# Performance work log

Measured on AMD Instinct MI355X. Metric: run time of the kernel, lower is better.

## Reference

```python
import jax, jax.numpy as jnp
import numpy as np

B, N, E, H = 16, 1024, 1024, 16  # batch must equal num_heads due to the 'hbkd' einsum in the original
D = E // H


def setup_inputs() -> dict:
    key = jax.random.key(0)
    ks = jax.random.split(key, 9)
    s = 0.02
    return {
        "x": jax.random.normal(ks[0], (B, N, E), dtype=jnp.float32),
        "Wq": jax.random.normal(ks[1], (E, E), dtype=jnp.float32) * s,
        "bq": jax.random.normal(ks[2], (E,), dtype=jnp.float32) * s,
        "Wk": jax.random.normal(ks[3], (E, E), dtype=jnp.float32) * s,
        "bk": jax.random.normal(ks[4], (E,), dtype=jnp.float32) * s,
        "Wv": jax.random.normal(ks[5], (E, E), dtype=jnp.float32) * s,
        "bv": jax.random.normal(ks[6], (E,), dtype=jnp.float32) * s,
        "Wp": jax.random.normal(ks[7], (E, E), dtype=jnp.float32) * s,
        "bp": jax.random.normal(ks[8], (E,), dtype=jnp.float32) * s,
    }


def _split_heads(t):  # [b, n, (h d)] -> [b, h, n, d]
    b, n, e = t.shape
    return t.reshape(b, n, H, D).transpose(0, 2, 1, 3)


def reference(x, Wq, bq, Wk, bk, Wv, bv, Wp, bp):
    q = _split_heads(x @ Wq.T + bq)  # [b, h, n, d]
    k = _split_heads(x @ Wk.T + bk)
    v = _split_heads(x @ Wv.T + bv)
    # Faithful to original: K is contracted with its batch/head axes SWAPPED ('hbkd').
    energy = jnp.einsum('bhqd,hbkd->bhqk', q, k)  # [b, h, n, n]
    # Faithful: softmax over the HEAD axis (dim=1), scale applied AFTER softmax.
    scale = E ** 0.5
    att = jax.nn.softmax(energy, axis=1) / scale
    # dropout rate is 0.0 -> identity
    o = jnp.einsum('bhal,bhlv->bhav', att, v)  # [b, h, n, d]
    o = o.transpose(0, 2, 1, 3).reshape(B, N, E)  # [b, n, (h d)]
    return o @ Wp.T + bp
```

## Files before the change

### kernel.cpp

```cpp
#include <hip/hip_runtime.h>
#include <hip/hip_bf16.h>

#define DEVI __device__ __forceinline__

typedef float f32x4 __attribute__((ext_vector_type(4)));
typedef short bf16x8 __attribute__((ext_vector_type(8)));
typedef unsigned short u16x4 __attribute__((ext_vector_type(4)));


DEVI unsigned short f2bf(float f) {
  union { float f; unsigned u; } v; v.f = f;
  unsigned r = v.u + 0x7fffu + ((v.u >> 16) & 1u);
  return (unsigned short)(r >> 16);
}

DEVI float fexp2(float x) {
#if __has_builtin(__builtin_amdgcn_exp2f)
  return __builtin_amdgcn_exp2f(x);
#else
  return exp2f(x);
#endif
}

DEVI float frcp(float x) {
#if __has_builtin(__builtin_amdgcn_rcpf)
  return __builtin_amdgcn_rcpf(x);
#else
  return 1.0f / x;
#endif
}

DEVI unsigned cvtpk(float a, float b) {
  unsigned r;
  asm("v_cvt_pk_bf16_f32 %0, %1, %2" : "=v"(r) : "v"(a), "v"(b));
  return r;
}

DEVI void gload_lds16(const unsigned short* g, unsigned short* l) {
  __builtin_amdgcn_global_load_lds(
      (const __attribute__((address_space(1))) void*)g,
      (__attribute__((address_space(3))) void*)l, 16, 0, 0);
}

DEVI void wg_barrier() {
  asm volatile("s_waitcnt lgkmcnt(0)" ::: "memory");
  __builtin_amdgcn_s_barrier();
  __builtin_amdgcn_sched_barrier(0);
}

__global__ void cvt_kernel(const float* __restrict__ s, unsigned short* __restrict__ d, int n4) {
  int i = blockIdx.x * blockDim.x + threadIdx.x;
  const int st = gridDim.x * blockDim.x;
  for (; i < n4; i += st) {
    const float4 v = reinterpret_cast<const float4*>(s)[i];
    u16x4 o;
    o[0] = f2bf(v.x); o[1] = f2bf(v.y); o[2] = f2bf(v.z); o[3] = f2bf(v.w);
    reinterpret_cast<u16x4*>(d)[i] = o;
  }
}

DEVI void gemm_tile(const unsigned short* __restrict__ A,
                    const unsigned short* __restrict__ Bw,
                    int m0, int n0,
                    unsigned short* lsA, unsigned short* lsB,
                    f32x4 acc[4][4]) {
  const int tid = threadIdx.x;
  const int w = tid >> 6, l = tid & 63, lg = l >> 4, lr = l & 15;
  const int wr = w >> 1, wc = w & 1;
  for (int kt = 0; kt < 1024; kt += 64) {
#pragma unroll
    for (int i = 0; i < 4; i++) {
      const int c = i * 256 + tid;
      const int row = c >> 3, col = (c & 7) * 8;
      gload_lds16(&A[(m0 + row) * 1024 + kt + col], &lsA[(i * 256 + w * 64) * 8]);
      gload_lds16(&Bw[(n0 + row) * 1024 + kt + col], &lsB[(i * 256 + w * 64) * 8]);
    }
    __syncthreads();
#pragma unroll
    for (int ks = 0; ks < 2; ks++) {
      bf16x8 af[4], bf_[4];
#pragma unroll
      for (int fi = 0; fi < 4; fi++) af[fi] = *(const bf16x8*)&lsA[(wr * 64 + fi * 16 + lr) * 64 + ks * 32 + lg * 8];
#pragma unroll
      for (int fj = 0; fj < 4; fj++) bf_[fj] = *(const bf16x8*)&lsB[(wc * 64 + fj * 16 + lr) * 64 + ks * 32 + lg * 8];
#pragma unroll
      for (int fi = 0; fi < 4; fi++)
#pragma unroll
        for (int fj = 0; fj < 4; fj++)
          acc[fi][fj] = __builtin_amdgcn_mfma_f32_16x16x32_bf16(af[fi], bf_[fj], acc[fi][fj], 0, 0, 0);
    }
    __syncthreads();
  }
}

__global__ __launch_bounds__(256, 2) void proj_qkv(
    const unsigned short* __restrict__ X, const unsigned short* __restrict__ W3,
    const float* __restrict__ bq, const float* __restrict__ bk, const float* __restrict__ bv,
    unsigned short* __restrict__ outq, unsigned short* __restrict__ outk, unsigned short* __restrict__ outv) {
  __shared__ unsigned short lsA[128 * 64];
  __shared__ unsigned short lsB[128 * 64];
  const int z = blockIdx.z;
  const int m0 = blockIdx.x * 128, n0 = blockIdx.y * 128;
  const unsigned short* Bw = W3 + z * 1048576;
  f32x4 acc[4][4];
  const f32x4 z4 = {0.f, 0.f, 0.f, 0.f};
#pragma unroll
  for (int i = 0; i < 4; i++)
#pragma unroll
    for (int j = 0; j < 4; j++) acc[i][j] = z4;
  gemm_tile(X, Bw, m0, n0, lsA, lsB, acc);

  const int tid = threadIdx.x;
  const int w = tid >> 6, l = tid & 63, lg = l >> 4, lr = l & 15, wr = w >> 1, wc = w & 1;
  const float* bias = (z == 0) ? bq : ((z == 1) ? bk : bv);
  const float SC = 1.4426950408889634f;
#pragma unroll
  for (int fi = 0; fi < 4; fi++) {
    const int mb = m0 + wr * 64 + fi * 16 + lg * 4;
#pragma unroll
    for (int fj = 0; fj < 4; fj++) {
      const int ncol = n0 + wc * 64 + fj * 16 + lr;
      const float bsv = bias[ncol];
      const int h = ncol >> 6, d = ncol & 63;
      if (z == 0) {
        const int ks = d >> 5, lgq = (d >> 3) & 3, eq = d & 7;
#pragma unroll
        for (int r = 0; r < 4; r++) {
          const int m = mb + r;
          const int bb = m >> 10, nr = m & 1023;
          const int nt = nr >> 4, lrq = nr & 15;
          const int idx = (((bb * 64 + nt) * 32 + h * 2 + ks) * 64 + lgq * 16 + lrq) * 8 + eq;
          outq[idx] = f2bf((acc[fi][fj][r] + bsv) * SC);
        }
      } else if (z == 1) {
        const int ks = d >> 5, lhi = ((d >> 3) & 3) * 16, eq = d & 7;
#pragma unroll
        for (int r = 0; r < 4; r++) {
          const int m = mb + r;
          const int n = m & 1023, bx = m >> 10;
          const int lane = lhi + (n & 15);
          const int idx = ((((h * 64 + (n >> 4)) * 16 + bx) * 2 + ks) * 64 + lane) * 8 + eq;
          outk[idx] = f2bf(acc[fi][fj][r] + bsv);
        }
      } else {
        const int dt = d >> 4, lrv = d & 15;
        const int bb = mb >> 10, n = mb & 1023;
        const int kc = n >> 5, lgv = (n >> 3) & 3, ev = n & 7;
        u16x4 pk;
#pragma unroll
        for (int r = 0; r < 4; r++) pk[r] = f2bf(acc[fi][fj][r] + bsv);
        const int idx0 = ((((bb * 16 + h) * 32 + kc) * 4 + dt) * 64 + lgv * 16 + lrv) * 8 + ev;
        *(u16x4*)&outv[idx0] = pk;
      }
    }
  }
}

__global__ __launch_bounds__(256, 2) void proj_out(
    const unsigned short* __restrict__ A, const unsigned short* __restrict__ Wp,
    const float* __restrict__ bias, float* __restrict__ out) {
  __shared__ unsigned short lsA[128 * 64];
  __shared__ unsigned short lsB[128 * 64];
  const int m0 = blockIdx.x * 128, n0 = blockIdx.y * 128;
  f32x4 acc[4][4];
  const f32x4 z4 = {0.f, 0.f, 0.f, 0.f};
#pragma unroll
  for (int i = 0; i < 4; i++)
#pragma unroll
    for (int j = 0; j < 4; j++) acc[i][j] = z4;
  gemm_tile(A, Wp, m0, n0, lsA, lsB, acc);
  const int tid = threadIdx.x;
  const int w = tid >> 6, l = tid & 63, lg = l >> 4, lr = l & 15, wr = w >> 1, wc = w & 1;
#pragma unroll
  for (int fi = 0; fi < 4; fi++) {
    const int mb = m0 + wr * 64 + fi * 16 + lg * 4;
#pragma unroll
    for (int fj = 0; fj < 4; fj++) {
      const int ncol = n0 + wc * 64 + fj * 16 + lr;
      const float bsv = bias[ncol];
#pragma unroll
      for (int r = 0; r < 4; r++) out[(mb + r) * 1024 + ncol] = acc[fi][fj][r] + bsv;
    }
  }
}

#define ATTN_BODY(IT, KC, KN)                                                  \
  {                                                                            \
    int qo = 0;                                                                \
    asm volatile("" : "+v"(qo));                                               \
    f32x4 e[4][2];                                                             \
    _Pragma("unroll") for (int hl = 0; hl < 4; hl++) {                         \
      const int h = hq * 4 + hl;                                               \
      _Pragma("unroll") for (int qh = 0; qh < 2; qh++) {                       \
        bf16x8 q0 = *(const bf16x8*)((const char*)qlds + qo + (qh * 32 + h * 2 + 0) * 1024 + l * 16); \
        bf16x8 q1 = *(const bf16x8*)((const char*)qlds + qo + (qh * 32 + h * 2 + 1) * 1024 + l * 16); \
        f32x4 t = __builtin_amdgcn_mfma_f32_16x16x32_bf16(KC[hl * 2 + 0], q0, z4, 0, 0, 0); \
        t = __builtin_amdgcn_mfma_f32_16x16x32_bf16(KC[hl * 2 + 1], q1, t, 0, 0, 0); \
        t[0] = fexp2(t[0]); t[1] = fexp2(t[1]); t[2] = fexp2(t[2]); t[3] = fexp2(t[3]); \
        e[hl][qh] = t;                                                         \
      }                                                                        \
    }                                                                          \
    {                                                                          \
      const unsigned short* knp = kroot + (size_t)((((IT) + 1) & 15) * 4) * 16384; \
      _Pragma("unroll") for (int i = 0; i < 8; i++) KN[i] = *(const bf16x8*)(knp + i * 512); \
    }                                                                          \
    f32x4 s0 = (e[0][0] + e[1][0]) + (e[2][0] + e[3][0]);                      \
    f32x4 s1 = (e[0][1] + e[1][1]) + (e[2][1] + e[3][1]);                      \
    *(f32x4*)&sumbuf[((ksub * 4 + hq) * 2 + 0) * 256 + l * 4] = s0;            \
    *(f32x4*)&sumbuf[((ksub * 4 + hq) * 2 + 1) * 256 + l * 4] = s1;            \
    wg_barrier();                                                              \
    _Pragma("unroll") for (int p = 1; p < 4; p++) {                            \
      const int hqp = hq ^ p;                                                  \
      s0 += *(const f32x4*)&sumbuf[((ksub * 4 + hqp) * 2 + 0) * 256 + l * 4];  \
      s1 += *(const f32x4*)&sumbuf[((ksub * 4 + hqp) * 2 + 1) * 256 + l * 4];  \
    }                                                                          \
    f32x4 inv0, inv1;                                                          \
    inv0[0] = frcp(s0[0]) * 0.03125f; inv0[1] = frcp(s0[1]) * 0.03125f;        \
    inv0[2] = frcp(s0[2]) * 0.03125f; inv0[3] = frcp(s0[3]) * 0.03125f;        \
    inv1[0] = frcp(s1[0]) * 0.03125f; inv1[1] = frcp(s1[1]) * 0.03125f;        \
    inv1[2] = frcp(s1[2]) * 0.03125f; inv1[3] = frcp(s1[3]) * 0.03125f;        \
    _Pragma("unroll") for (int hl = 0; hl < 4; hl++) {                         \
      const int h = hq * 4 + hl;                                               \
      _Pragma("unroll") for (int qh = 0; qh < 2; qh++) {                       \
        f32x4 vv = e[hl][qh] * (qh ? inv1 : inv0);                             \
        uint2 pk;                                                              \
        pk.x = cvtpk(vv[0], vv[1]);                                            \
        pk.y = cvtpk(vv[2], vv[3]);                                            \
        *(uint2*)((char*)abuf + h * 4096 + (qh * 16 + lr) * 128 + ((kpart ^ wswz) << 1)) = pk; \
      }                                                                        \
    }                                                                          \
    {                                                                          \
      const unsigned short* vbp = vroot + (size_t)((IT) * 2) * 2048;           \
      _Pragma("unroll") for (int kst = 0; kst < 2; kst++)                      \
        _Pragma("unroll") for (int dt = 0; dt < 4; dt++)                       \
          vr[kst * 4 + dt] = *(const bf16x8*)(vbp + kst * 2048 + dt * 512);    \
    }                                                                          \
    wg_barrier();                                                              \
    bf16x8 pa[2][2];                                                           \
    _Pragma("unroll") for (int qt = 0; qt < 2; qt++)                           \
      _Pragma("unroll") for (int kst = 0; kst < 2; kst++)                      \
        pa[qt][kst] = *(const bf16x8*)((const char*)abuf + w * 4096 + qt * 2048 + lr * 128 + (((kst * 4 + lg) ^ (lr & 7)) << 4)); \
    _Pragma("unroll") for (int qt = 0; qt < 2; qt++)                           \
      _Pragma("unroll") for (int kst = 0; kst < 2; kst++)                      \
        _Pragma("unroll") for (int dt = 0; dt < 4; dt++)                       \
          oacc[qt][dt] = __builtin_amdgcn_mfma_f32_16x16x32_bf16(pa[qt][kst], vr[kst * 4 + dt], oacc[qt][dt], 0, 0, 0); \
  }

__global__ __launch_bounds__(1024, 4) void attn5(
    const unsigned short* __restrict__ Q2,
    const unsigned short* __restrict__ K2,
    const unsigned short* __restrict__ V2,
    unsigned short* __restrict__ O) {
  __shared__ unsigned short qlds[32768];
  __shared__ unsigned short abuf[32768];
  __shared__ float sumbuf[8192];

  const int tid = threadIdx.x;
  const int w = tid >> 6, l = tid & 63;
  const int lr = l & 15, lg = l >> 4;
  const int bid = blockIdx.x;
  const int swz = (bid & 7) * 64 + (bid >> 3);
  const int b = swz >> 5, qt32 = swz & 31;
  const int ksub = w & 3, hq = w >> 2;

  {
    const unsigned short* qsrc = Q2 + (size_t)(b * 64 + qt32 * 2) * 16384 + tid * 8;
    unsigned short* qdst = qlds + tid * 8;
#pragma unroll
    for (int r = 0; r < 4; r++) gload_lds16(qsrc + r * 8192, qdst + r * 8192);
  }

  const int kpart = ksub * 16 + lg * 4;
  const int wswz = (lr & 7) << 3;

  const f32x4 z4 = {0.f, 0.f, 0.f, 0.f};
  f32x4 oacc[2][4];
#pragma unroll
  for (int qt = 0; qt < 2; qt++)
#pragma unroll
    for (int dt = 0; dt < 4; dt++) oacc[qt][dt] = z4;

  const unsigned short* kroot = K2 + (size_t)(b * 64 + ksub) * 16384 + hq * 4096 + l * 8;
  const unsigned short* vroot = V2 + (size_t)((b * 16 + w) * 32) * 2048 + l * 8;

  bf16x8 kA[8], kB[8], vr[8];
#pragma unroll
  for (int i = 0; i < 8; i++) kA[i] = *(const bf16x8*)(kroot + i * 512);

  asm volatile("s_waitcnt vmcnt(0) lgkmcnt(0)" ::: "memory");
  __builtin_amdgcn_s_barrier();
  __builtin_amdgcn_sched_barrier(0);

#pragma unroll 1
  for (int it2 = 0; it2 < 8; it2++) {
    ATTN_BODY(it2 * 2, kA, kB)
    ATTN_BODY(it2 * 2 + 1, kB, kA)
  }

#pragma unroll
  for (int qt = 0; qt < 2; qt++)
#pragma unroll
    for (int dt = 0; dt < 4; dt++)
#pragma unroll
      for (int r = 0; r < 4; r++) {
        const int n = qt32 * 32 + qt * 16 + lg * 4 + r;
        O[(size_t)(b * 1024 + n) * 1024 + w * 64 + dt * 16 + lr] = f2bf(oacc[qt][dt][r]);
      }
}

extern "C" void kernel_launch(void* const* d_in, const int* in_sizes, int n_in,
                              void* d_out, int out_size, void* d_ws, size_t ws_size,
                              hipStream_t stream) {
  const float* x  = (const float*)d_in[0];
  const float* Wq = (const float*)d_in[1];
  const float* bq = (const float*)d_in[2];
  const float* Wk = (const float*)d_in[3];
  const float* bk = (const float*)d_in[4];
  const float* Wv = (const float*)d_in[5];
  const float* bv = (const float*)d_in[6];
  const float* Wp = (const float*)d_in[7];
  const float* bp = (const float*)d_in[8];

  char* ws = (char*)d_ws;
  unsigned short* xbf  = (unsigned short*)(ws);
  unsigned short* qbf  = (unsigned short*)(ws + 33554432);
  unsigned short* kbf  = (unsigned short*)(ws + 67108864);
  unsigned short* vtbf = (unsigned short*)(ws + 100663296);
  unsigned short* wbf  = (unsigned short*)(ws + 134217728);

  cvt_kernel<<<2048, 256, 0, stream>>>(x, xbf, 4194304);
  cvt_kernel<<<512, 256, 0, stream>>>(Wq, wbf, 262144);
  cvt_kernel<<<512, 256, 0, stream>>>(Wk, wbf + 1048576, 262144);
  cvt_kernel<<<512, 256, 0, stream>>>(Wv, wbf + 2097152, 262144);
  cvt_kernel<<<512, 256, 0, stream>>>(Wp, wbf + 3145728, 262144);

  proj_qkv<<<dim3(128, 8, 3), 256, 0, stream>>>(xbf, wbf, bq, bk, bv, qbf, kbf, vtbf);
  attn5<<<512, 1024, 0, stream>>>(qbf, kbf, vtbf, xbf);
  proj_out<<<dim3(128, 8, 1), 256, 0, stream>>>(xbf, wbf + 3145728, bp, (float*)d_out);
}
```

Measured before the change: 350.3 us.

## Software-pipeline attention loop: overlap PV MFMA of previous tile with next energy phase

Restructures the attention kernel loop so the P·V matrix multiply for iteration it-1 is issued alongside the QK energy/exp phase of iteration it, with a prologue and epilogue. K fragments are now loaded just-in-time inside the energy phase instead of double-buffered in registers, and V is loaded at the start of each iteration. PV MFMAs get raised wave priority via s_setprio. This aims to hide barrier and latency stalls between the softmax reduction and PV, but direct K loads may expose global-memory latency that the old register double-buffering hid.

```diff
diff --git a/kernel.cpp b/kernel.cpp
--- a/kernel.cpp
+++ b/kernel.cpp
@@ -184,31 +184,32 @@
   }
 }
 
-#define ATTN_BODY(IT, KC, KN)                                                  \
+#define E_PHASE(IT)                                                            \
   {                                                                            \
     int qo = 0;                                                                \
     asm volatile("" : "+v"(qo));                                               \
-    f32x4 e[4][2];                                                             \
+    const unsigned short* kp = kroot + (size_t)(IT) * 65536;                   \
     _Pragma("unroll") for (int hl = 0; hl < 4; hl++) {                         \
       const int h = hq * 4 + hl;                                               \
+      bf16x8 k0 = *(const bf16x8*)(kp + (hl * 2 + 0) * 512);                   \
+      bf16x8 k1 = *(const bf16x8*)(kp + (hl * 2 + 1) * 512);                   \
       _Pragma("unroll") for (int qh = 0; qh < 2; qh++) {                       \
         bf16x8 q0 = *(const bf16x8*)((const char*)qlds + qo + (qh * 32 + h * 2 + 0) * 1024 + l * 16); \
         bf16x8 q1 = *(const bf16x8*)((const char*)qlds + qo + (qh * 32 + h * 2 + 1) * 1024 + l * 16); \
-        f32x4 t = __builtin_amdgcn_mfma_f32_16x16x32_bf16(KC[hl * 2 + 0], q0, z4, 0, 0, 0); \
-        t = __builtin_amdgcn_mfma_f32_16x16x32_bf16(KC[hl * 2 + 1], q1, t, 0, 0, 0); \
+        f32x4 t = __builtin_amdgcn_mfma_f32_16x16x32_bf16(k0, q0, z4, 0, 0, 0); \
+        t = __builtin_amdgcn_mfma_f32_16x16x32_bf16(k1, q1, t, 0, 0, 0);       \
         t[0] = fexp2(t[0]); t[1] = fexp2(t[1]); t[2] = fexp2(t[2]); t[3] = fexp2(t[3]); \
         e[hl][qh] = t;                                                         \
       }                                                                        \
     }                                                                          \
-    {                                                                          \
-      const unsigned short* knp = kroot + (size_t)((((IT) + 1) & 15) * 4) * 16384; \
-      _Pragma("unroll") for (int i = 0; i < 8; i++) KN[i] = *(const bf16x8*)(knp + i * 512); \
-    }                                                                          \
-    f32x4 s0 = (e[0][0] + e[1][0]) + (e[2][0] + e[3][0]);                      \
-    f32x4 s1 = (e[0][1] + e[1][1]) + (e[2][1] + e[3][1]);                      \
+    s0 = (e[0][0] + e[1][0]) + (e[2][0] + e[3][0]);                            \
+    s1 = (e[0][1] + e[1][1]) + (e[2][1] + e[3][1]);                            \
     *(f32x4*)&sumbuf[((ksub * 4 + hq) * 2 + 0) * 256 + l * 4] = s0;            \
     *(f32x4*)&sumbuf[((ksub * 4 + hq) * 2 + 1) * 256 + l * 4] = s1;            \
-    wg_barrier();                                                              \
+  }
+
+#define FINISH_PHASE()                                                         \
+  {                                                                            \
     _Pragma("unroll") for (int p = 1; p < 4; p++) {                            \
       const int hqp = hq ^ p;                                                  \
       s0 += *(const f32x4*)&sumbuf[((ksub * 4 + hqp) * 2 + 0) * 256 + l * 4];  \
@@ -229,24 +230,33 @@
         *(uint2*)((char*)abuf + h * 4096 + (qh * 16 + lr) * 128 + ((kpart ^ wswz) << 1)) = pk; \
       }                                                                        \
     }                                                                          \
-    {                                                                          \
-      const unsigned short* vbp = vroot + (size_t)((IT) * 2) * 2048;           \
-      _Pragma("unroll") for (int kst = 0; kst < 2; kst++)                      \
-        _Pragma("unroll") for (int dt = 0; dt < 4; dt++)                       \
-          vr[kst * 4 + dt] = *(const bf16x8*)(vbp + kst * 2048 + dt * 512);    \
-    }                                                                          \
-    wg_barrier();                                                              \
-    bf16x8 pa[2][2];                                                           \
+  }
+
+#define V_LOAD(IT)                                                             \
+  {                                                                            \
+    const unsigned short* vbp = vroot + (size_t)(IT) * 4096;                   \
+    _Pragma("unroll") for (int f = 0; f < 8; f++)                              \
+      vr[f] = *(const bf16x8*)(vbp + f * 512);                                 \
+  }
+
+#define PA_LOAD()                                                              \
+  {                                                                            \
     _Pragma("unroll") for (int qt = 0; qt < 2; qt++)                           \
       _Pragma("unroll") for (int kst = 0; kst < 2; kst++)                      \
-        pa[qt][kst] = *(const bf16x8*)((const char*)abuf + w * 4096 + qt * 2048 + lr * 128 + (((kst * 4 + lg) ^ (lr & 7)) << 4)); \
+        pa[qt * 2 + kst] = *(const bf16x8*)((const char*)abuf + w * 4096 + qt * 2048 + lr * 128 + (((kst * 4 + lg) ^ (lr & 7)) << 4)); \
+  }
+
+#define PV_PHASE()                                                             \
+  {                                                                            \
+    __builtin_amdgcn_s_setprio(1);                                             \
     _Pragma("unroll") for (int qt = 0; qt < 2; qt++)                           \
       _Pragma("unroll") for (int kst = 0; kst < 2; kst++)                      \
         _Pragma("unroll") for (int dt = 0; dt < 4; dt++)                       \
-          oacc[qt][dt] = __builtin_amdgcn_mfma_f32_16x16x32_bf16(pa[qt][kst], vr[kst * 4 + dt], oacc[qt][dt], 0, 0, 0); \
-  }
-
-__global__ __launch_bounds__(1024, 4) void attn5(
+          oacc[qt][dt] = __builtin_amdgcn_mfma_f32_16x16x32_bf16(pa[qt * 2 + kst], vr[kst * 4 + dt], oacc[qt][dt], 0, 0, 0); \
+    __builtin_amdgcn_s_setprio(0);                                             \
+  }
+
+__global__ __launch_bounds__(1024, 4) void attn6(
     const unsigned short* __restrict__ Q2,
     const unsigned short* __restrict__ K2,
     const unsigned short* __restrict__ V2,
@@ -283,19 +293,33 @@
   const unsigned short* kroot = K2 + (size_t)(b * 64 + ksub) * 16384 + hq * 4096 + l * 8;
   const unsigned short* vroot = V2 + (size_t)((b * 16 + w) * 32) * 2048 + l * 8;
 
-  bf16x8 kA[8], kB[8], vr[8];
-#pragma unroll
-  for (int i = 0; i < 8; i++) kA[i] = *(const bf16x8*)(kroot + i * 512);
+  f32x4 e[4][2];
+  f32x4 s0, s1;
+  bf16x8 vr[8], pa[4];
 
   asm volatile("s_waitcnt vmcnt(0) lgkmcnt(0)" ::: "memory");
   __builtin_amdgcn_s_barrier();
   __builtin_amdgcn_sched_barrier(0);
 
+  E_PHASE(0)
+  wg_barrier();
+  FINISH_PHASE()
+  wg_barrier();
+  PA_LOAD()
+
 #pragma unroll 1
-  for (int it2 = 0; it2 < 8; it2++) {
-    ATTN_BODY(it2 * 2, kA, kB)
-    ATTN_BODY(it2 * 2 + 1, kB, kA)
-  }
+  for (int it = 1; it < 16; it++) {
+    V_LOAD(it - 1)
+    E_PHASE(it)
+    PV_PHASE()
+    wg_barrier();
+    FINISH_PHASE()
+    wg_barrier();
+    PA_LOAD()
+  }
+
+  V_LOAD(15)
+  PV_PHASE()
 
 #pragma unroll
   for (int qt = 0; qt < 2; qt++)
@@ -335,6 +359,6 @@
   cvt_kernel<<<512, 256, 0, stream>>>(Wp, wbf + 3145728, 262144);
 
   proj_qkv<<<dim3(128, 8, 3), 256, 0, stream>>>(xbf, wbf, bq, bk, bv, qbf, kbf, vtbf);
-  attn5<<<512, 1024, 0, stream>>>(qbf, kbf, vtbf, xbf);
+  attn6<<<512, 1024, 0, stream>>>(qbf, kbf, vtbf, xbf);
   proj_out<<<dim3(128, 8, 1), 256, 0, stream>>>(xbf, wbf + 3145728, bp, (float*)d_out);
 }
```

Result: slower. 391.0 us (+11.6%).

## Rewrite projection GEMMs as 256x256 double-buffered, swizzled, pipelined tiles

Applied to the files above, without the earlier changes.

Replaces the 128x128 single-buffered GEMM tile used by the QKV and output projections with a 256x256 tile computed by 512 threads. Global-to-LDS loads for the next K-step are interleaved with MFMA phases across two LDS buffers, gated by vmcnt waits and s_setprio. An XOR swizzle on LDS columns is meant to avoid bank conflicts. The goal is to hide memory latency and raise arithmetic intensity, at the cost of 128 KB of LDS per block, higher register pressure and fewer blocks in the grid.

```diff
diff --git a/kernel.cpp b/kernel.cpp
--- a/kernel.cpp
+++ b/kernel.cpp
@@ -59,67 +59,111 @@
   }
 }
 
-DEVI void gemm_tile(const unsigned short* __restrict__ A,
-                    const unsigned short* __restrict__ Bw,
-                    int m0, int n0,
-                    unsigned short* lsA, unsigned short* lsB,
-                    f32x4 acc[4][4]) {
+
+#define STA(BUF, C, K0) gload_lds16(&A[(size_t)(m0 + (C)*64 + srow) * 1024 + (K0) + scol], &lsA[BUF][(C)*4096 + tid*8])
+#define STB(BUF, C, K0) gload_lds16(&Bw[(size_t)(n0 + (C)*64 + srow) * 1024 + (K0) + scol], &lsB[BUF][(C)*4096 + tid*8])
+
+#define DSREAD_A(BUF, MF, KS) (*(const bf16x8*)&lsA[BUF][arow + (MF)*1024 + ((KS) ? sx1 : sx0)])
+#define DSREAD_B(BUF, NF, KS) (*(const bf16x8*)&lsB[BUF][brow + (NF)*1024 + ((KS) ? sx1 : sx0)])
+
+#define MFMA16(P, AF)                                                          \
+    __builtin_amdgcn_s_setprio(1);                                             \
+    _Pragma("unroll") for (int mfi = 0; mfi < 2; mfi++)                        \
+      _Pragma("unroll") for (int nf = 0; nf < 4; nf++)                         \
+        _Pragma("unroll") for (int ks = 0; ks < 2; ks++)                       \
+          acc[2*(P)+mfi][nf] = __builtin_amdgcn_mfma_f32_16x16x32_bf16(        \
+              AF[mfi][ks], bfr[nf][ks], acc[2*(P)+mfi][nf], 0, 0, 0);          \
+    __builtin_amdgcn_s_setprio(0);
+
+#define PHASE(BUF, P, LB, STG)                                                 \
+  { __builtin_amdgcn_s_barrier();                                              \
+    bf16x8 af[2][2];                                                           \
+    _Pragma("unroll") for (int i = 0; i < 2; i++)                              \
+      _Pragma("unroll") for (int k2 = 0; k2 < 2; k2++)                         \
+        af[i][k2] = DSREAD_A(BUF, 2*(P)+i, k2);                                \
+    if (LB) {                                                                  \
+      _Pragma("unroll") for (int n2 = 0; n2 < 4; n2++)                         \
+        _Pragma("unroll") for (int k2 = 0; k2 < 2; k2++)                       \
+          bfr[n2][k2] = DSREAD_B(BUF, n2, k2);                                 \
+    }                                                                          \
+    STG;                                                                       \
+    MFMA16(P, af) }
+
+#define GSTEP(CB, NB, K1)                                                      \
+    asm volatile("s_waitcnt vmcnt(2)" ::: "memory");                           \
+    PHASE(CB, 0, 1, { STB(NB,0,K1); STB(NB,1,K1); })                           \
+    PHASE(CB, 1, 0, { STB(NB,2,K1); STB(NB,3,K1); })                           \
+    asm volatile("s_waitcnt vmcnt(4)" ::: "memory");                           \
+    PHASE(CB, 2, 0, { STA(NB,0,K1); STA(NB,2,K1); })                           \
+    PHASE(CB, 3, 0, { STA(NB,1,K1); STA(NB,3,K1); })
+
+DEVI void gemm256_main(const unsigned short* __restrict__ A,
+                       const unsigned short* __restrict__ Bw,
+                       int m0, int n0,
+                       unsigned short (&lsA)[2][16384],
+                       unsigned short (&lsB)[2][16384],
+                       f32x4 (&acc)[8][4]) {
   const int tid = threadIdx.x;
-  const int w = tid >> 6, l = tid & 63, lg = l >> 4, lr = l & 15;
-  const int wr = w >> 1, wc = w & 1;
-  for (int kt = 0; kt < 1024; kt += 64) {
-#pragma unroll
-    for (int i = 0; i < 4; i++) {
-      const int c = i * 256 + tid;
-      const int row = c >> 3, col = (c & 7) * 8;
-      gload_lds16(&A[(m0 + row) * 1024 + kt + col], &lsA[(i * 256 + w * 64) * 8]);
-      gload_lds16(&Bw[(n0 + row) * 1024 + kt + col], &lsB[(i * 256 + w * 64) * 8]);
-    }
-    __syncthreads();
-#pragma unroll
-    for (int ks = 0; ks < 2; ks++) {
-      bf16x8 af[4], bf_[4];
-#pragma unroll
-      for (int fi = 0; fi < 4; fi++) af[fi] = *(const bf16x8*)&lsA[(wr * 64 + fi * 16 + lr) * 64 + ks * 32 + lg * 8];
-#pragma unroll
-      for (int fj = 0; fj < 4; fj++) bf_[fj] = *(const bf16x8*)&lsB[(wc * 64 + fj * 16 + lr) * 64 + ks * 32 + lg * 8];
-#pragma unroll
-      for (int fi = 0; fi < 4; fi++)
-#pragma unroll
-        for (int fj = 0; fj < 4; fj++)
-          acc[fi][fj] = __builtin_amdgcn_mfma_f32_16x16x32_bf16(af[fi], bf_[fj], acc[fi][fj], 0, 0, 0);
-    }
-    __syncthreads();
-  }
-}
-
-__global__ __launch_bounds__(256, 2) void proj_qkv(
-    const unsigned short* __restrict__ X, const unsigned short* __restrict__ W3,
+  const int l = tid & 63, lr = l & 15, lg = l >> 4;
+  const int w = tid >> 6, wm = w >> 2, wn = w & 3;
+  const int srow = tid >> 3;
+  const int scol = (((tid & 7) ^ (srow & 7)) * 8);
+  const int sx0 = (lg * 8) ^ ((lr & 7) << 3);
+  const int sx1 = (32 + lg * 8) ^ ((lr & 7) << 3);
+  const int arow = (wm * 128 + lr) * 64;
+  const int brow = (wn * 64 + lr) * 64;
+
+  STB(0,0,0); STB(0,1,0); STB(0,2,0); STB(0,3,0);
+  STA(0,0,0); STA(0,1,0); STA(0,2,0); STA(0,3,0);
+  asm volatile("s_waitcnt vmcnt(0)" ::: "memory");
+  __builtin_amdgcn_s_barrier();
+
+  bf16x8 bfr[4][2];
+
+#pragma unroll 1
+  for (int t7 = 0; t7 < 7; ++t7) {
+    const int k1 = t7 * 128 + 64;
+    GSTEP(0, 1, k1)
+    GSTEP(1, 0, k1 + 64)
+  }
+  GSTEP(0, 1, 960)
+  asm volatile("s_waitcnt vmcnt(2)" ::: "memory");
+  PHASE(1, 0, 1, {})
+  PHASE(1, 1, 0, {})
+  asm volatile("s_waitcnt vmcnt(0)" ::: "memory");
+  PHASE(1, 2, 0, {})
+  PHASE(1, 3, 0, {})
+}
+
+__global__ __launch_bounds__(512, 2) void proj_qkv8(
+    const unsigned short* __restrict__ A, const unsigned short* __restrict__ W3,
     const float* __restrict__ bq, const float* __restrict__ bk, const float* __restrict__ bv,
     unsigned short* __restrict__ outq, unsigned short* __restrict__ outk, unsigned short* __restrict__ outv) {
-  __shared__ unsigned short lsA[128 * 64];
-  __shared__ unsigned short lsB[128 * 64];
+  __shared__ unsigned short lsA[2][16384];
+  __shared__ unsigned short lsB[2][16384];
   const int z = blockIdx.z;
-  const int m0 = blockIdx.x * 128, n0 = blockIdx.y * 128;
+  const int m0 = blockIdx.x * 256, n0 = blockIdx.y * 256;
   const unsigned short* Bw = W3 + z * 1048576;
-  f32x4 acc[4][4];
+  f32x4 acc[8][4];
   const f32x4 z4 = {0.f, 0.f, 0.f, 0.f};
 #pragma unroll
-  for (int i = 0; i < 4; i++)
+  for (int i = 0; i < 8; i++)
 #pragma unroll
     for (int j = 0; j < 4; j++) acc[i][j] = z4;
-  gemm_tile(X, Bw, m0, n0, lsA, lsB, acc);
+
+  gemm256_main(A, Bw, m0, n0, lsA, lsB, acc);
 
   const int tid = threadIdx.x;
-  const int w = tid >> 6, l = tid & 63, lg = l >> 4, lr = l & 15, wr = w >> 1, wc = w & 1;
+  const int l = tid & 63, lr = l & 15, lg = l >> 4;
+  const int w = tid >> 6, wm = w >> 2, wn = w & 3;
   const float* bias = (z == 0) ? bq : ((z == 1) ? bk : bv);
   const float SC = 1.4426950408889634f;
 #pragma unroll
-  for (int fi = 0; fi < 4; fi++) {
-    const int mb = m0 + wr * 64 + fi * 16 + lg * 4;
-#pragma unroll
-    for (int fj = 0; fj < 4; fj++) {
-      const int ncol = n0 + wc * 64 + fj * 16 + lr;
+  for (int mf = 0; mf < 8; mf++) {
+    const int mb = m0 + wm * 128 + mf * 16 + lg * 4;
+#pragma unroll
+    for (int nf = 0; nf < 4; nf++) {
+      const int ncol = n0 + wn * 64 + nf * 16 + lr;
       const float bsv = bias[ncol];
       const int h = ncol >> 6, d = ncol & 63;
       if (z == 0) {
@@ -130,7 +174,7 @@
           const int bb = m >> 10, nr = m & 1023;
           const int nt = nr >> 4, lrq = nr & 15;
           const int idx = (((bb * 64 + nt) * 32 + h * 2 + ks) * 64 + lgq * 16 + lrq) * 8 + eq;
-          outq[idx] = f2bf((acc[fi][fj][r] + bsv) * SC);
+          outq[idx] = f2bf((acc[mf][nf][r] + bsv) * SC);
         }
       } else if (z == 1) {
         const int ks = d >> 5, lhi = ((d >> 3) & 3) * 16, eq = d & 7;
@@ -140,7 +184,7 @@
           const int n = m & 1023, bx = m >> 10;
           const int lane = lhi + (n & 15);
           const int idx = ((((h * 64 + (n >> 4)) * 16 + bx) * 2 + ks) * 64 + lane) * 8 + eq;
-          outk[idx] = f2bf(acc[fi][fj][r] + bsv);
+          outk[idx] = f2bf(acc[mf][nf][r] + bsv);
         }
       } else {
         const int dt = d >> 4, lrv = d & 15;
@@ -148,7 +192,7 @@
         const int kc = n >> 5, lgv = (n >> 3) & 3, ev = n & 7;
         u16x4 pk;
 #pragma unroll
-        for (int r = 0; r < 4; r++) pk[r] = f2bf(acc[fi][fj][r] + bsv);
+        for (int r = 0; r < 4; r++) pk[r] = f2bf(acc[mf][nf][r] + bsv);
         const int idx0 = ((((bb * 16 + h) * 32 + kc) * 4 + dt) * 64 + lgv * 16 + lrv) * 8 + ev;
         *(u16x4*)&outv[idx0] = pk;
       }
@@ -156,30 +200,33 @@
   }
 }
 
-__global__ __launch_bounds__(256, 2) void proj_out(
+__global__ __launch_bounds__(512, 2) void proj_out8(
     const unsigned short* __restrict__ A, const unsigned short* __restrict__ Wp,
     const float* __restrict__ bias, float* __restrict__ out) {
-  __shared__ unsigned short lsA[128 * 64];
-  __shared__ unsigned short lsB[128 * 64];
-  const int m0 = blockIdx.x * 128, n0 = blockIdx.y * 128;
-  f32x4 acc[4][4];
+  __shared__ unsigned short lsA[2][16384];
+  __shared__ unsigned short lsB[2][16384];
+  const int m0 = blockIdx.x * 256, n0 = blockIdx.y * 256;
+  f32x4 acc[8][4];
   const f32x4 z4 = {0.f, 0.f, 0.f, 0.f};
 #pragma unroll
-  for (int i = 0; i < 4; i++)
+  for (int i = 0; i < 8; i++)
 #pragma unroll
     for (int j = 0; j < 4; j++) acc[i][j] = z4;
-  gemm_tile(A, Wp, m0, n0, lsA, lsB, acc);
+
+  gemm256_main(A, Wp, m0, n0, lsA, lsB, acc);
+
   const int tid = threadIdx.x;
-  const int w = tid >> 6, l = tid & 63, lg = l >> 4, lr = l & 15, wr = w >> 1, wc = w & 1;
-#pragma unroll
-  for (int fi = 0; fi < 4; fi++) {
-    const int mb = m0 + wr * 64 + fi * 16 + lg * 4;
-#pragma unroll
-    for (int fj = 0; fj < 4; fj++) {
-      const int ncol = n0 + wc * 64 + fj * 16 + lr;
+  const int l = tid & 63, lr = l & 15, lg = l >> 4;
+  const int w = tid >> 6, wm = w >> 2, wn = w & 3;
+#pragma unroll
+  for (int mf = 0; mf < 8; mf++) {
+    const int mb = m0 + wm * 128 + mf * 16 + lg * 4;
+#pragma unroll
+    for (int nf = 0; nf < 4; nf++) {
+      const int ncol = n0 + wn * 64 + nf * 16 + lr;
       const float bsv = bias[ncol];
 #pragma unroll
-      for (int r = 0; r < 4; r++) out[(mb + r) * 1024 + ncol] = acc[fi][fj][r] + bsv;
+      for (int r = 0; r < 4; r++) out[(size_t)(mb + r) * 1024 + ncol] = acc[mf][nf][r] + bsv;
     }
   }
 }
@@ -334,7 +381,7 @@
   cvt_kernel<<<512, 256, 0, stream>>>(Wv, wbf + 2097152, 262144);
   cvt_kernel<<<512, 256, 0, stream>>>(Wp, wbf + 3145728, 262144);
 
-  proj_qkv<<<dim3(128, 8, 3), 256, 0, stream>>>(xbf, wbf, bq, bk, bv, qbf, kbf, vtbf);
+  proj_qkv8<<<dim3(64, 4, 3), 512, 0, stream>>>(xbf, wbf, bq, bk, bv, qbf, kbf, vtbf);
   attn5<<<512, 1024, 0, stream>>>(qbf, kbf, vtbf, xbf);
-  proj_out<<<dim3(128, 8, 1), 256, 0, stream>>>(xbf, wbf + 3145728, bp, (float*)d_out);
-}
+  proj_out8<<<dim3(64, 4, 1), 512, 0, stream>>>(xbf, wbf + 3145728, bp, (float*)d_out);
+}
```

Measured after the change: 330.7 us. 1.06x faster.
